# Kernel tuning notes

Hardware: AMD Instinct MI355X
Metric: run time of the kernel (lower is better)

## Reference

```python
import jax, jax.numpy as jnp
import numpy as np

EMB = 768
HEADS = 12


def setup_inputs() -> dict:
    key = jax.random.key(0)
    ks = jax.random.split(key, 5)
    B, N, E = 8, 1024, EMB
    x = jax.random.normal(ks[0], (B, N, E), dtype=jnp.float32)
    s = 1.0 / np.sqrt(E)
    W_qkv = jax.random.normal(ks[1], (E, 3 * E), dtype=jnp.float32) * s
    b_qkv = jnp.zeros((3 * E,), dtype=jnp.float32)
    W_fc = jax.random.normal(ks[2], (E, E), dtype=jnp.float32) * s
    b_fc = jnp.zeros((E,), dtype=jnp.float32)
    return {"x": x, "W_qkv": W_qkv, "b_qkv": b_qkv, "W_fc": W_fc, "b_fc": b_fc}


def reference(x, W_qkv, b_qkv, W_fc, b_fc):
    B, N, E = x.shape
    H = HEADS
    D = E // H
    qkv = x @ W_qkv + b_qkv                      # [B, N, 3E]
    q, k, v = jnp.split(qkv, 3, axis=-1)
    # b n (h d) -> b h n d
    def to_heads(t):
        return t.reshape(B, N, H, D).transpose(0, 2, 1, 3)
    q, k, v = to_heads(q), to_heads(k), to_heads(v)
    scale = 1.0 / jnp.sqrt(jnp.float32(E))       # NOTE: scales by sqrt(emb_size), not head dim
    attn = jnp.einsum('bhid,bhjd->bhij', q, k) * scale
    attn = jax.nn.softmax(attn, axis=-1)
    out = jnp.einsum('bhij,bhjd->bhid', attn, v)
    out = out.transpose(0, 2, 1, 3).reshape(B, N, E)  # b h n d -> b n (h d)
    return out @ W_fc + b_fc
```

## Files before the change

### kernel.cpp

```cpp
#include <hip/hip_runtime.h>


typedef unsigned short u16;
typedef unsigned int u32;
typedef __attribute__((ext_vector_type(8))) short short8;
typedef __attribute__((ext_vector_type(4))) float f32x4;

#define DEV static __device__ __forceinline__

DEV u16 f2bf(float f) {
  union { float f; u32 u; } v; v.f = f;
  return (u16)((v.u + 0x7FFFu + ((v.u >> 16) & 1u)) >> 16);
}

DEV void gload_lds16(const void* g, void* l) {
  __builtin_amdgcn_global_load_lds(
      (const __attribute__((address_space(1))) void*)g,
      (__attribute__((address_space(3))) void*)l, 16, 0, 0);
}

__global__ void cvt_bf16_kernel(const float* __restrict__ in, u16* __restrict__ out, int n8) {
  int idx = blockIdx.x * blockDim.x + threadIdx.x;
  int stride = gridDim.x * blockDim.x;
  for (int i = idx; i < n8; i += stride) {
    float4 a = reinterpret_cast<const float4*>(in)[2 * i];
    float4 b = reinterpret_cast<const float4*>(in)[2 * i + 1];
    uint4 o;
    o.x = f2bf(a.x) | ((u32)f2bf(a.y) << 16);
    o.y = f2bf(a.z) | ((u32)f2bf(a.w) << 16);
    o.z = f2bf(b.x) | ((u32)f2bf(b.y) << 16);
    o.w = f2bf(b.z) | ((u32)f2bf(b.w) << 16);
    reinterpret_cast<uint4*>(out)[i] = o;
  }
}

__global__ void trcvt_kernel(const float* __restrict__ in, u16* __restrict__ out,
                             int K, int Nn) {
  __shared__ u16 tile[64][72];
  int ntiles = Nn >> 6;
  int tk = blockIdx.x / ntiles, tn = blockIdx.x % ntiles;
  int k0 = tk << 6, n0 = tn << 6;
  int t = threadIdx.x;
  int r = t >> 4;
  int c4 = (t & 15) << 2;
#pragma unroll
  for (int ps = 0; ps < 4; ++ps) {
    int k = r + ps * 16;
    float4 v = *reinterpret_cast<const float4*>(&in[(size_t)(k0 + k) * Nn + n0 + c4]);
    tile[c4 + 0][k] = f2bf(v.x);
    tile[c4 + 1][k] = f2bf(v.y);
    tile[c4 + 2][k] = f2bf(v.z);
    tile[c4 + 3][k] = f2bf(v.w);
  }
  __syncthreads();
  int nr = t >> 3;
  int c8 = (t & 7) << 3;
#pragma unroll
  for (int ps = 0; ps < 2; ++ps) {
    int n = nr + ps * 32;
    uint4 v = *reinterpret_cast<const uint4*>(&tile[n][c8]);
    *reinterpret_cast<uint4*>(&out[(size_t)(n0 + n) * K + k0 + c8]) = v;
  }
}

__global__ void trv_kernel(const u16* __restrict__ vh, u16* __restrict__ vt) {
  __shared__ u16 tile[64][72];
  int nt = blockIdx.x & 15;
  int bh = blockIdx.x >> 4;
  int n0 = nt << 6;
  int t = threadIdx.x;
  int nr = t >> 3;
  int d8 = (t & 7) << 3;
  const u16* src = vh + ((size_t)bh * 1024 + n0) * 64;
#pragma unroll
  for (int ps = 0; ps < 2; ++ps) {
    int n = nr + ps * 32;
    uint4 v = *reinterpret_cast<const uint4*>(&src[(size_t)n * 64 + d8]);
    const u16* e = reinterpret_cast<const u16*>(&v);
#pragma unroll
    for (int j = 0; j < 8; ++j) tile[d8 + j][n] = e[j];
  }
  __syncthreads();
  u16* dst = vt + ((size_t)bh * 64) * 1024 + n0;
#pragma unroll
  for (int ps = 0; ps < 2; ++ps) {
    int d = nr + ps * 32;
    uint4 v = *reinterpret_cast<const uint4*>(&tile[d][d8]);
    *reinterpret_cast<uint4*>(&dst[(size_t)d * 1024 + d8]) = v;
  }
}

template <int MODE>
__global__ __launch_bounds__(256, 2) void gemm_bt(
    const u16* __restrict__ A, const u16* __restrict__ Bt,
    const float* __restrict__ bias, void* __restrict__ Cout,
    u16* __restrict__ qh, u16* __restrict__ kh, u16* __restrict__ vh,
    int Mm, int Nn, int Kk) {
  __shared__ u16 As[128 * 32];
  __shared__ u16 Bs[128 * 32];
  const int nTiles = Nn >> 7;
  const int tm = blockIdx.x / nTiles, tn = blockIdx.x % nTiles;
  const int m0 = tm << 7, n0 = tn << 7;
  const int tid = threadIdx.x;
  const int w = tid >> 6, lane = tid & 63;
  const int g = lane >> 4, p = lane & 15;
  const int wr = w >> 1, wc = w & 1;
  const int lrow = lane >> 2;
  const int lcol = (lane & 3) << 3;

  f32x4 acc[4][4] = {};

  for (int kt = 0; kt < Kk; kt += 32) {
#pragma unroll
    for (int i = 0; i < 2; ++i) {
      int trow = w * 32 + i * 16;
      gload_lds16(A + (size_t)(m0 + trow + lrow) * Kk + kt + lcol, &As[trow * 32]);
      gload_lds16(Bt + (size_t)(n0 + trow + lrow) * Kk + kt + lcol, &Bs[trow * 32]);
    }
    __syncthreads();
    short8 af[4], bf[4];
#pragma unroll
    for (int mb = 0; mb < 4; ++mb)
      af[mb] = *reinterpret_cast<const short8*>(&As[(wr * 64 + mb * 16 + p) * 32 + g * 8]);
#pragma unroll
    for (int nb = 0; nb < 4; ++nb)
      bf[nb] = *reinterpret_cast<const short8*>(&Bs[(wc * 64 + nb * 16 + p) * 32 + g * 8]);
#pragma unroll
    for (int mb = 0; mb < 4; ++mb)
#pragma unroll
      for (int nb = 0; nb < 4; ++nb)
        acc[mb][nb] = __builtin_amdgcn_mfma_f32_16x16x32_bf16(af[mb], bf[nb], acc[mb][nb], 0, 0, 0);
    __syncthreads();
  }

  const float qscale = 0.036084391824351615f;
#pragma unroll
  for (int nb = 0; nb < 4; ++nb) {
    int ncol = n0 + wc * 64 + nb * 16 + p;
    float bv = bias[ncol];
    if (MODE == 0) {
#pragma unroll
      for (int mb = 0; mb < 4; ++mb)
#pragma unroll
        for (int r = 0; r < 4; ++r) {
          int m = m0 + wr * 64 + mb * 16 + g * 4 + r;
          ((float*)Cout)[(size_t)m * Nn + ncol] = acc[mb][nb][r] + bv;
        }
    } else {
      int h64 = ncol >> 6;
      int which = h64 / 12;
      int hh = h64 - which * 12;
      int d = nb * 16 + p;
      u16* dst = which == 0 ? qh : (which == 1 ? kh : vh);
      float sc = which == 0 ? qscale : 1.f;
#pragma unroll
      for (int mb = 0; mb < 4; ++mb)
#pragma unroll
        for (int r = 0; r < 4; ++r) {
          int m = m0 + wr * 64 + mb * 16 + g * 4 + r;
          int bb = m >> 10, nr = m & 1023;
          dst[(((size_t)bb * 12 + hh) * 1024 + nr) * 64 + d] = f2bf((acc[mb][nb][r] + bv) * sc);
        }
    }
  }
}

__global__ __launch_bounds__(512, 6) void attn_kernel(
    const u16* __restrict__ qh, const u16* __restrict__ kh,
    const u16* __restrict__ vt, u16* __restrict__ ao) {
  __shared__ u16 Ks[2][64 * 64];
  __shared__ u16 Vs[2][64 * 64];
  __shared__ u16 Ps[8][16 * 64];
  const int bid = blockIdx.x;
  const int qt = bid & 7;
  const int bh = bid >> 3;
  const int b = bh / 12, h = bh % 12;
  const int tid = threadIdx.x;
  const int w = tid >> 6, lane = tid & 63;
  const int g = lane >> 4, p = lane & 15;
  const int qrow = qt * 128 + w * 16;

  const u16* qbase = qh + ((size_t)bh * 1024 + qrow + p) * 64;
  short8 qf0 = *reinterpret_cast<const short8*>(qbase + g * 8);
  short8 qf1 = *reinterpret_cast<const short8*>(qbase + 32 + g * 8);

  const int ci = w * 64 + lane;
  const int crow = ci >> 3;
  const int csw = (ci & 7) ^ (crow & 7);
  const u16* ksrc = kh + (((size_t)bh * 1024 + crow) << 6) + csw * 8;
  const u16* vsrc = vt + ((size_t)bh * 64 + crow) * 1024 + csw * 8;
  u16* myp = Ps[w];

  const int sw = p & 7;
  const int c0 = (g ^ sw) << 3;
  const int c1 = ((4 + g) ^ sw) << 3;

  float m_run = -1e30f, l_run = 0.f;
  f32x4 oacc[4] = {};

  gload_lds16(ksrc, &Ks[0][w * 512]);
  gload_lds16(vsrc, &Vs[0][w * 512]);
  __syncthreads();

  int buf = 0;
  for (int kt = 0; kt < 1024; kt += 64) {
    if (kt < 960) {
      gload_lds16(ksrc + ((kt + 64) << 6), &Ks[buf ^ 1][w * 512]);
      gload_lds16(vsrc + (kt + 64), &Vs[buf ^ 1][w * 512]);
    }

    f32x4 s[4];
    __builtin_amdgcn_s_setprio(1);
#pragma unroll
    for (int jb = 0; jb < 4; ++jb) {
      const u16* kb = &Ks[buf][(jb * 16 + p) * 64];
      short8 k0 = *reinterpret_cast<const short8*>(kb + c0);
      short8 k1 = *reinterpret_cast<const short8*>(kb + c1);
      f32x4 z = {};
      z = __builtin_amdgcn_mfma_f32_16x16x32_bf16(k0, qf0, z, 0, 0, 0);
      z = __builtin_amdgcn_mfma_f32_16x16x32_bf16(k1, qf1, z, 0, 0, 0);
      s[jb] = z;
    }
    __builtin_amdgcn_s_setprio(0);

    float tmax = -1e30f;
#pragma unroll
    for (int jb = 0; jb < 4; ++jb)
#pragma unroll
      for (int r = 0; r < 4; ++r) tmax = fmaxf(tmax, s[jb][r]);
    tmax = fmaxf(tmax, __shfl_xor(tmax, 16));
    tmax = fmaxf(tmax, __shfl_xor(tmax, 32));
    float m_new = fmaxf(m_run, tmax);
    float alpha = __expf(m_run - m_new);
    float lsum = 0.f;
#pragma unroll
    for (int jb = 0; jb < 4; ++jb)
#pragma unroll
      for (int r = 0; r < 4; ++r) {
        float e = __expf(s[jb][r] - m_new);
        s[jb][r] = e;
        lsum += e;
      }
    lsum += __shfl_xor(lsum, 16);
    lsum += __shfl_xor(lsum, 32);
    l_run = l_run * alpha + lsum;
    m_run = m_new;

#pragma unroll
    for (int jb = 0; jb < 4; ++jb) {
      uint2 pk;
      pk.x = f2bf(s[jb][0]) | ((u32)f2bf(s[jb][1]) << 16);
      pk.y = f2bf(s[jb][2]) | ((u32)f2bf(s[jb][3]) << 16);
      int c = 2 * jb + (g >> 1);
      *reinterpret_cast<uint2*>(&myp[p * 64 + ((c ^ sw) << 3) + ((g & 1) << 2)]) = pk;
    }

    float al[4];
#pragma unroll
    for (int r = 0; r < 4; ++r) al[r] = __shfl(alpha, g * 4 + r);
#pragma unroll
    for (int nb = 0; nb < 4; ++nb)
#pragma unroll
      for (int r = 0; r < 4; ++r) oacc[nb][r] *= al[r];

    short8 pa0 = *reinterpret_cast<const short8*>(&myp[p * 64 + c0]);
    short8 pa1 = *reinterpret_cast<const short8*>(&myp[p * 64 + c1]);
    __builtin_amdgcn_s_setprio(1);
#pragma unroll
    for (int nb = 0; nb < 4; ++nb) {
      const u16* vb = &Vs[buf][(nb * 16 + p) * 64];
      short8 v0 = *reinterpret_cast<const short8*>(vb + c0);
      short8 v1 = *reinterpret_cast<const short8*>(vb + c1);
      oacc[nb] = __builtin_amdgcn_mfma_f32_16x16x32_bf16(pa0, v0, oacc[nb], 0, 0, 0);
      oacc[nb] = __builtin_amdgcn_mfma_f32_16x16x32_bf16(pa1, v1, oacc[nb], 0, 0, 0);
    }
    __builtin_amdgcn_s_setprio(0);

    __syncthreads();
    buf ^= 1;
  }

  float li[4];
#pragma unroll
  for (int r = 0; r < 4; ++r) li[r] = 1.f / __shfl(l_run, g * 4 + r);
  u16* obase = ao + ((size_t)(b * 1024 + qrow)) * 768 + h * 64;
#pragma unroll
  for (int nb = 0; nb < 4; ++nb)
#pragma unroll
    for (int r = 0; r < 4; ++r)
      obase[(size_t)(g * 4 + r) * 768 + nb * 16 + p] = f2bf(oacc[nb][r] * li[r]);
}

extern "C" void kernel_launch(void* const* d_in, const int* in_sizes, int n_in,
                              void* d_out, int out_size, void* d_ws, size_t ws_size,
                              hipStream_t stream) {
  const float* x = (const float*)d_in[0];
  const float* Wqkv = (const float*)d_in[1];
  const float* bqkv = (const float*)d_in[2];
  const float* Wfc = (const float*)d_in[3];
  const float* bfc = (const float*)d_in[4];
  float* out = (float*)d_out;

  char* ws = (char*)d_ws;
  u16* xb    = (u16*)(ws);
  u16* wqkvT = (u16*)(ws + 12582912);
  u16* wfcT  = (u16*)(ws + 16121856);
  u16* qh    = (u16*)(ws + 17301504);
  u16* kh    = (u16*)(ws + 29884416);
  u16* vh    = (u16*)(ws + 42467328);
  u16* vt    = (u16*)(ws + 55050240);
  u16* ao    = (u16*)(ws + 67633152);

  cvt_bf16_kernel<<<2048, 256, 0, stream>>>(x, xb, (8192 * 768) / 8);
  trcvt_kernel<<<12 * 36, 256, 0, stream>>>(Wqkv, wqkvT, 768, 2304);
  trcvt_kernel<<<12 * 12, 256, 0, stream>>>(Wfc, wfcT, 768, 768);
  gemm_bt<2><<<64 * 18, 256, 0, stream>>>(xb, wqkvT, bqkv, nullptr, qh, kh, vh, 8192, 2304, 768);
  trv_kernel<<<96 * 16, 256, 0, stream>>>(vh, vt);
  attn_kernel<<<96 * 8, 512, 0, stream>>>(qh, kh, vt, ao);
  gemm_bt<0><<<64 * 6, 256, 0, stream>>>(ao, wfcT, bfc, out, nullptr, nullptr, nullptr, 8192, 768, 768);
}
```

Baseline: 147.0 us.

## Rewrite GEMM as 8-wave 256x128 tile with triple-buffered swizzled LDS pipeline

Replaces the 4-wave 128x128 GEMM with an 8-wave kernel that computes 256x128 tiles using K=64 steps. Global-to-LDS loads are triple-buffered two steps ahead and XOR-swizzled to avoid bank conflicts, and the workgroup index is remapped for cache locality. MFMA bursts are interleaved with LDS reads and guarded by explicit barriers, waitcnt and setprio. The goal is to hide memory latency and raise MFMA utilization, at the cost of much more LDS per block (lower occupancy), a hardcoded K=768, and fragile hand-written synchronization.

```diff
diff --git a/kernel.cpp b/kernel.cpp
--- a/kernel.cpp
+++ b/kernel.cpp
@@ -91,47 +91,105 @@
 }
 
 template <int MODE>
-__global__ __launch_bounds__(256, 2) void gemm_bt(
+__global__ __launch_bounds__(512, 2) void gemm8p(
     const u16* __restrict__ A, const u16* __restrict__ Bt,
     const float* __restrict__ bias, void* __restrict__ Cout,
     u16* __restrict__ qh, u16* __restrict__ kh, u16* __restrict__ vh,
-    int Mm, int Nn, int Kk) {
-  __shared__ u16 As[128 * 32];
-  __shared__ u16 Bs[128 * 32];
-  const int nTiles = Nn >> 7;
-  const int tm = blockIdx.x / nTiles, tn = blockIdx.x % nTiles;
-  const int m0 = tm << 7, n0 = tn << 7;
+    int Nn) {
+  __shared__ u16 As[3][256 * 64];
+  __shared__ u16 Bs[3][128 * 64];
+  const int nTn = Nn >> 7;
+  const int nwg = gridDim.x;
+  int wg = blockIdx.x;
+  wg = (wg & 7) * (nwg >> 3) + (wg >> 3);
+  const int tm = wg / nTn, tn = wg % nTn;
+  const int m0 = tm << 8, n0 = tn << 7;
   const int tid = threadIdx.x;
   const int w = tid >> 6, lane = tid & 63;
   const int g = lane >> 4, p = lane & 15;
-  const int wr = w >> 1, wc = w & 1;
-  const int lrow = lane >> 2;
-  const int lcol = (lane & 3) << 3;
+  const int wr = w & 3, wc = w >> 2;
+
+  const int srow = lane >> 3;
+  const int schunk = (lane & 7) ^ srow;
+  const u16* Asrc = A + (size_t)(m0 + w * 8 + srow) * 768 + schunk * 8;
+  const u16* Bsrc = Bt + (size_t)(n0 + w * 8 + srow) * 768 + schunk * 8;
+  const int c0 = ((0 + g) ^ (p & 7)) << 3;
+  const int c1 = ((4 + g) ^ (p & 7)) << 3;
 
   f32x4 acc[4][4] = {};
 
-  for (int kt = 0; kt < Kk; kt += 32) {
-#pragma unroll
-    for (int i = 0; i < 2; ++i) {
-      int trow = w * 32 + i * 16;
-      gload_lds16(A + (size_t)(m0 + trow + lrow) * Kk + kt + lcol, &As[trow * 32]);
-      gload_lds16(Bt + (size_t)(n0 + trow + lrow) * Kk + kt + lcol, &Bs[trow * 32]);
-    }
-    __syncthreads();
-    short8 af[4], bf[4];
-#pragma unroll
-    for (int mb = 0; mb < 4; ++mb)
-      af[mb] = *reinterpret_cast<const short8*>(&As[(wr * 64 + mb * 16 + p) * 32 + g * 8]);
-#pragma unroll
-    for (int nb = 0; nb < 4; ++nb)
-      bf[nb] = *reinterpret_cast<const short8*>(&Bs[(wc * 64 + nb * 16 + p) * 32 + g * 8]);
-#pragma unroll
-    for (int mb = 0; mb < 4; ++mb)
-#pragma unroll
-      for (int nb = 0; nb < 4; ++nb)
-        acc[mb][nb] = __builtin_amdgcn_mfma_f32_16x16x32_bf16(af[mb], bf[nb], acc[mb][nb], 0, 0, 0);
-    __syncthreads();
-  }
+#define STAGE_A(k, j, s) \
+  gload_lds16(Asrc + (size_t)(j) * 64 * 768 + (k) * 64, &As[s][((j) * 64 + w * 8) * 64])
+#define STAGE_B(k, j, s) \
+  gload_lds16(Bsrc + (size_t)(j) * 64 * 768 + (k) * 64, &Bs[s][((j) * 64 + w * 8) * 64])
+
+  STAGE_A(0, 0, 0); STAGE_A(0, 1, 0); STAGE_B(0, 0, 0);
+  STAGE_A(0, 2, 0); STAGE_A(0, 3, 0); STAGE_B(0, 1, 0);
+  STAGE_A(1, 0, 1); STAGE_A(1, 1, 1); STAGE_B(1, 0, 1);
+  STAGE_A(1, 2, 1); STAGE_A(1, 3, 1); STAGE_B(1, 1, 1);
+  asm volatile("s_waitcnt vmcnt(6)");
+  __builtin_amdgcn_sched_barrier(0);
+  __builtin_amdgcn_s_barrier();
+
+#pragma unroll
+  for (int k = 0; k < 12; ++k) {
+    const int s = k % 3;
+    const int sn = (k + 2) % 3;
+    const u16* as = As[s];
+    const u16* bs = Bs[s];
+    short8 bfr[4][2], afr[2][2];
+#pragma unroll
+    for (int nb = 0; nb < 4; ++nb) {
+      const u16* rb = bs + (wc * 64 + nb * 16 + p) * 64;
+      bfr[nb][0] = *reinterpret_cast<const short8*>(rb + c0);
+      bfr[nb][1] = *reinterpret_cast<const short8*>(rb + c1);
+    }
+#pragma unroll
+    for (int mb = 0; mb < 2; ++mb) {
+      const u16* ra = as + (wr * 64 + mb * 16 + p) * 64;
+      afr[mb][0] = *reinterpret_cast<const short8*>(ra + c0);
+      afr[mb][1] = *reinterpret_cast<const short8*>(ra + c1);
+    }
+    if (k < 10) { STAGE_A(k + 2, 0, sn); STAGE_A(k + 2, 1, sn); STAGE_B(k + 2, 0, sn); }
+    __builtin_amdgcn_s_barrier();
+    asm volatile("s_waitcnt lgkmcnt(0)");
+    __builtin_amdgcn_sched_barrier(0);
+    __builtin_amdgcn_s_setprio(1);
+#pragma unroll
+    for (int mb = 0; mb < 2; ++mb)
+#pragma unroll
+      for (int nb = 0; nb < 4; ++nb) {
+        acc[mb][nb] = __builtin_amdgcn_mfma_f32_16x16x32_bf16(afr[mb][0], bfr[nb][0], acc[mb][nb], 0, 0, 0);
+        acc[mb][nb] = __builtin_amdgcn_mfma_f32_16x16x32_bf16(afr[mb][1], bfr[nb][1], acc[mb][nb], 0, 0, 0);
+      }
+    __builtin_amdgcn_s_setprio(0);
+    __builtin_amdgcn_s_barrier();
+#pragma unroll
+    for (int mb = 0; mb < 2; ++mb) {
+      const u16* ra = as + (wr * 64 + (mb + 2) * 16 + p) * 64;
+      afr[mb][0] = *reinterpret_cast<const short8*>(ra + c0);
+      afr[mb][1] = *reinterpret_cast<const short8*>(ra + c1);
+    }
+    if (k < 10) { STAGE_A(k + 2, 2, sn); STAGE_A(k + 2, 3, sn); STAGE_B(k + 2, 1, sn); }
+    __builtin_amdgcn_s_barrier();
+    asm volatile("s_waitcnt lgkmcnt(0)");
+    __builtin_amdgcn_sched_barrier(0);
+    __builtin_amdgcn_s_setprio(1);
+#pragma unroll
+    for (int mb = 0; mb < 2; ++mb)
+#pragma unroll
+      for (int nb = 0; nb < 4; ++nb) {
+        acc[mb + 2][nb] = __builtin_amdgcn_mfma_f32_16x16x32_bf16(afr[mb][0], bfr[nb][0], acc[mb + 2][nb], 0, 0, 0);
+        acc[mb + 2][nb] = __builtin_amdgcn_mfma_f32_16x16x32_bf16(afr[mb][1], bfr[nb][1], acc[mb + 2][nb], 0, 0, 0);
+      }
+    __builtin_amdgcn_s_setprio(0);
+    if (k < 10) asm volatile("s_waitcnt vmcnt(6)");
+    else if (k == 10) asm volatile("s_waitcnt vmcnt(0)");
+    __builtin_amdgcn_sched_barrier(0);
+    __builtin_amdgcn_s_barrier();
+  }
+#undef STAGE_A
+#undef STAGE_B
 
   const float qscale = 0.036084391824351615f;
 #pragma unroll
@@ -151,6 +209,7 @@
       int which = h64 / 12;
       int hh = h64 - which * 12;
       int d = nb * 16 + p;
+      d = ncol & 63;
       u16* dst = which == 0 ? qh : (which == 1 ? kh : vh);
       float sc = which == 0 ? qscale : 1.f;
 #pragma unroll
@@ -314,8 +373,8 @@
   cvt_bf16_kernel<<<2048, 256, 0, stream>>>(x, xb, (8192 * 768) / 8);
   trcvt_kernel<<<12 * 36, 256, 0, stream>>>(Wqkv, wqkvT, 768, 2304);
   trcvt_kernel<<<12 * 12, 256, 0, stream>>>(Wfc, wfcT, 768, 768);
-  gemm_bt<2><<<64 * 18, 256, 0, stream>>>(xb, wqkvT, bqkv, nullptr, qh, kh, vh, 8192, 2304, 768);
+  gemm8p<2><<<576, 512, 0, stream>>>(xb, wqkvT, bqkv, nullptr, qh, kh, vh, 2304);
   trv_kernel<<<96 * 16, 256, 0, stream>>>(vh, vt);
   attn_kernel<<<96 * 8, 512, 0, stream>>>(qh, kh, vt, ao);
-  gemm_bt<0><<<64 * 6, 256, 0, stream>>>(ao, wfcT, bfc, out, nullptr, nullptr, nullptr, 8192, 768, 768);
-}
+  gemm8p<0><<<192, 512, 0, stream>>>(ao, wfcT, bfc, out, nullptr, nullptr, nullptr, 768);
+}
```

Result: no change. 147.7 us (+0.5%).

## Rewrite GEMM with triple-buffered LDS pipeline, 256x128 tiles, swizzle and XCD remap

Applied to the files above, without the earlier changes.

Replaces the synchronous double-barrier GEMM loop with a three-stage LDS ring where global-to-LDS loads for tile k+2 are issued while MFMAs run on tile k, using explicit waitcnt and barriers. Block tile grows to 256x128 with 512 threads, LDS chunks are XOR-swizzled to avoid bank conflicts, and block IDs are remapped across 8 XCDs to improve L2 locality. K is hardcoded to 768 and the grid size changes. The intent is to hide global load latency in both projection GEMMs, at the cost of more LDS use and lower occupancy.

```diff
diff --git a/kernel.cpp b/kernel.cpp
--- a/kernel.cpp
+++ b/kernel.cpp
@@ -91,47 +91,78 @@
 }
 
 template <int MODE>
-__global__ __launch_bounds__(256, 2) void gemm_bt(
+__global__ __launch_bounds__(512, 4) void gemm_fp(
     const u16* __restrict__ A, const u16* __restrict__ Bt,
     const float* __restrict__ bias, void* __restrict__ Cout,
     u16* __restrict__ qh, u16* __restrict__ kh, u16* __restrict__ vh,
-    int Mm, int Nn, int Kk) {
-  __shared__ u16 As[128 * 32];
-  __shared__ u16 Bs[128 * 32];
-  const int nTiles = Nn >> 7;
-  const int tm = blockIdx.x / nTiles, tn = blockIdx.x % nTiles;
-  const int m0 = tm << 7, n0 = tn << 7;
+    int Nn) {
+  __shared__ u16 As[3][256 * 32];
+  __shared__ u16 Bs[3][128 * 32];
+  const int nTn = Nn >> 7;
+  const int nwg = gridDim.x;
+  int wg = blockIdx.x;
+  wg = (wg & 7) * (nwg >> 3) + (wg >> 3);
+  const int tm = wg / nTn, tn = wg % nTn;
+  const int m0 = tm << 8, n0 = tn << 7;
   const int tid = threadIdx.x;
   const int w = tid >> 6, lane = tid & 63;
   const int g = lane >> 4, p = lane & 15;
-  const int wr = w >> 1, wc = w & 1;
-  const int lrow = lane >> 2;
-  const int lcol = (lane & 3) << 3;
+  const int wr = w & 3, wc = w >> 2;
+
+  const int srow = lane >> 2;
+  const int schunk = (lane & 3) ^ (srow & 3);
+  const u16* Asrc = A + (size_t)(m0 + w * 32 + srow) * 768 + schunk * 8;
+  const u16* Bsrc = Bt + (size_t)(n0 + w * 16 + srow) * 768 + schunk * 8;
+  const int csw = (g ^ (p & 3)) << 3;
 
   f32x4 acc[4][4] = {};
 
-  for (int kt = 0; kt < Kk; kt += 32) {
-#pragma unroll
-    for (int i = 0; i < 2; ++i) {
-      int trow = w * 32 + i * 16;
-      gload_lds16(A + (size_t)(m0 + trow + lrow) * Kk + kt + lcol, &As[trow * 32]);
-      gload_lds16(Bt + (size_t)(n0 + trow + lrow) * Kk + kt + lcol, &Bs[trow * 32]);
-    }
-    __syncthreads();
+#define STAGE(kt, s)                                                        \
+  do {                                                                      \
+    gload_lds16(Asrc + (size_t)(kt) * 32, &As[s][(w * 32) * 32]);           \
+    gload_lds16(Asrc + (size_t)(kt) * 32 + 16 * 768, &As[s][(w * 32 + 16) * 32]); \
+    gload_lds16(Bsrc + (size_t)(kt) * 32, &Bs[s][(w * 16) * 32]);           \
+  } while (0)
+
+  STAGE(0, 0);
+  STAGE(1, 1);
+  STAGE(2, 2);
+  asm volatile("s_waitcnt vmcnt(6)" ::: "memory");
+  __builtin_amdgcn_sched_barrier(0);
+  __builtin_amdgcn_s_barrier();
+
+  int s = 0;
+  for (int k = 0; k < 24; ++k) {
+    const u16* as = As[s];
+    const u16* bs = Bs[s];
     short8 af[4], bf[4];
 #pragma unroll
     for (int mb = 0; mb < 4; ++mb)
-      af[mb] = *reinterpret_cast<const short8*>(&As[(wr * 64 + mb * 16 + p) * 32 + g * 8]);
+      af[mb] = *reinterpret_cast<const short8*>(&as[(wr * 64 + mb * 16 + p) * 32 + csw]);
 #pragma unroll
     for (int nb = 0; nb < 4; ++nb)
-      bf[nb] = *reinterpret_cast<const short8*>(&Bs[(wc * 64 + nb * 16 + p) * 32 + g * 8]);
+      bf[nb] = *reinterpret_cast<const short8*>(&bs[(wc * 64 + nb * 16 + p) * 32 + csw]);
+    if (k < 22) {
+      int sn = s + 2; if (sn >= 3) sn -= 3;
+      STAGE(k + 2, sn);
+    }
+    __builtin_amdgcn_s_barrier();
+    asm volatile("s_waitcnt lgkmcnt(0)" ::: "memory");
+    __builtin_amdgcn_sched_barrier(0);
+    __builtin_amdgcn_s_setprio(1);
 #pragma unroll
     for (int mb = 0; mb < 4; ++mb)
 #pragma unroll
       for (int nb = 0; nb < 4; ++nb)
         acc[mb][nb] = __builtin_amdgcn_mfma_f32_16x16x32_bf16(af[mb], bf[nb], acc[mb][nb], 0, 0, 0);
-    __syncthreads();
-  }
+    __builtin_amdgcn_s_setprio(0);
+    if (k < 22) asm volatile("s_waitcnt vmcnt(3)" ::: "memory");
+    else if (k == 22) asm volatile("s_waitcnt vmcnt(0)" ::: "memory");
+    __builtin_amdgcn_sched_barrier(0);
+    __builtin_amdgcn_s_barrier();
+    ++s; if (s >= 3) s = 0;
+  }
+#undef STAGE
 
   const float qscale = 0.036084391824351615f;
 #pragma unroll
@@ -150,7 +181,7 @@
       int h64 = ncol >> 6;
       int which = h64 / 12;
       int hh = h64 - which * 12;
-      int d = nb * 16 + p;
+      int d = ncol & 63;
       u16* dst = which == 0 ? qh : (which == 1 ? kh : vh);
       float sc = which == 0 ? qscale : 1.f;
 #pragma unroll
@@ -314,8 +345,8 @@
   cvt_bf16_kernel<<<2048, 256, 0, stream>>>(x, xb, (8192 * 768) / 8);
   trcvt_kernel<<<12 * 36, 256, 0, stream>>>(Wqkv, wqkvT, 768, 2304);
   trcvt_kernel<<<12 * 12, 256, 0, stream>>>(Wfc, wfcT, 768, 768);
-  gemm_bt<2><<<64 * 18, 256, 0, stream>>>(xb, wqkvT, bqkv, nullptr, qh, kh, vh, 8192, 2304, 768);
+  gemm_fp<2><<<576, 512, 0, stream>>>(xb, wqkvT, bqkv, nullptr, qh, kh, vh, 2304);
   trv_kernel<<<96 * 16, 256, 0, stream>>>(vh, vt);
   attn_kernel<<<96 * 8, 512, 0, stream>>>(qh, kh, vt, ao);
-  gemm_bt<0><<<64 * 6, 256, 0, stream>>>(ao, wfcT, bfc, out, nullptr, nullptr, nullptr, 8192, 768, 768);
-}
+  gemm_fp<0><<<192, 512, 0, stream>>>(ao, wfcT, bfc, out, nullptr, nullptr, nullptr, 768);
+}
```

Measured after the change: 138.7 us. -5.6%, faster.
